# Performance work log

Hardware: AMD Instinct MI355X
Metric: run time of the kernel (lower is better)

Reference implementation:

```python
import jax, jax.numpy as jnp
import numpy as np

MARGIN = 0.3


def setup_inputs() -> dict:
    key = jax.random.key(0)
    k1, k2 = jax.random.split(key)
    N, D, C = 8192, 512, 1024
    embeddings = jax.random.normal(k1, (N, D), dtype=jnp.float32)
    labels = jax.random.randint(k2, (N,), 0, C, dtype=jnp.int64)
    return {"embeddings": embeddings, "labels": labels}


def reference(embeddings, labels):
    # L2-normalize rows, cosine distance via Gram matrix: d = 1 - e_i . e_j
    e = embeddings / jnp.linalg.norm(embeddings, axis=1, keepdims=True)
    dist = 1.0 - jnp.matmul(e, e.T)  # [N, N]

    same = labels[:, None] == labels[None, :]           # [N, N] bool
    eye = jnp.eye(labels.shape[0], dtype=bool)
    pos_mask = same & ~eye                              # positives exclude self
    neg_mask = ~same                                    # negatives

    # Batch-hard mining: hardest (farthest) positive, hardest (closest) negative
    hardest_pos = jnp.max(jnp.where(pos_mask, dist, -jnp.inf), axis=1)
    hardest_neg = jnp.min(jnp.where(neg_mask, dist, jnp.inf), axis=1)

    loss = jax.nn.relu(hardest_pos - hardest_neg + MARGIN)
    return jnp.mean(loss)
```

## Files before the change

kernel.cpp:

```cpp
#include <hip/hip_runtime.h>
#include <hip/hip_fp8.h>
#include <hip/hip_fp16.h>
#include <stdint.h>

#define MARGIN 0.3f

constexpr int N = 8192;
constexpr int D = 512;
constexpr int BM = 128, BN = 128;
constexpr int NKS = D / 64;
constexpr int NT = N / BM;
constexpr int NPAIR = NT * (NT + 1) / 2;
constexpr int WEDGE = NPAIR / 8;
constexpr float ESCALE = 16.0f;
constexpr float INV_SC2 = 1.0f / (ESCALE * ESCALE);

typedef int i32x8 __attribute__((ext_vector_type(8)));
typedef float f32x16 __attribute__((ext_vector_type(16)));
typedef __fp16 h2 __attribute__((ext_vector_type(2)));

constexpr unsigned INF2 = 0x7C007C00u;

__device__ __forceinline__ unsigned char f2fp8(float f) {
  return __hip_fp8_e4m3(f).__x;
}

__device__ __forceinline__ unsigned pkmin(unsigned a, unsigned b) {
  unsigned d;
  asm("v_pk_min_f16 %0, %1, %2" : "=v"(d) : "v"(a), "v"(b));
  return d;
}

__device__ __forceinline__ unsigned cvtpk(float lo, float hi) {
  union { h2 h; unsigned u; } cv;
  cv.h = __builtin_amdgcn_cvt_pkrtz(lo, hi);
  return cv.u;
}

__device__ __forceinline__ void pair_from_q(int q, int& ti, int& tj) {
  int SI = 0;
  while (32 * (SI + 1) * (SI + 1) + 4 * (SI + 1) <= q) ++SI;
  int r = q - (32 * SI * SI + 4 * SI);
  int i, j, SJ;
  if (r < 64 * SI) {
    SJ = r >> 6;
    int w = r & 63;
    i = w >> 3;
    j = w & 7;
  } else {
    int d = r - 64 * SI;
    SJ = SI;
    i = 0;
    while ((i + 1) * (i + 2) / 2 <= d) ++i;
    j = d - i * (i + 1) / 2;
  }
  ti = SI * 8 + i;
  tj = SJ * 8 + j;
}


__global__ __launch_bounds__(256) void normalize_rows(
    const float* __restrict__ emb, unsigned char* __restrict__ e8,
    float* __restrict__ out) {
  if (blockIdx.x == 0 && threadIdx.x == 0) out[0] = 0.f;
  const int wave = threadIdx.x >> 6, lane = threadIdx.x & 63;
  const int row = blockIdx.x * 4 + wave;
  const float4* src = (const float4*)(emb + (size_t)row * D);
  float4 x0 = src[lane];
  float4 x1 = src[lane + 64];
  float ss = x0.x * x0.x + x0.y * x0.y + x0.z * x0.z + x0.w * x0.w +
             x1.x * x1.x + x1.y * x1.y + x1.z * x1.z + x1.w * x1.w;
#pragma unroll
  for (int m = 1; m < 64; m <<= 1) ss += __shfl_xor(ss, m, 64);
  const float r = rsqrtf(ss) * ESCALE;
  union { unsigned char b[8]; uint2 u; } o;
  o.b[0] = f2fp8(x0.x * r); o.b[1] = f2fp8(x0.y * r);
  o.b[2] = f2fp8(x0.z * r); o.b[3] = f2fp8(x0.w * r);
  o.b[4] = f2fp8(x1.x * r); o.b[5] = f2fp8(x1.y * r);
  o.b[6] = f2fp8(x1.z * r); o.b[7] = f2fp8(x1.w * r);
  const int n = row & 31;
  const unsigned inner =
      (unsigned)(n * 32) + ((unsigned)((lane >> 2) & 1)) * 1024 + (lane & 3) * 8;
  const unsigned off = (unsigned)((row >> 5) * 8 + (lane >> 3)) * 2048 + inner;
  *(uint2*)(e8 + off) = o.u;
}

__global__ __launch_bounds__(256, 3) void bh_gemm_sym(
    const unsigned char* __restrict__ e8, const int* __restrict__ labels,
    unsigned* __restrict__ scr) {
  __shared__ unsigned bufR[2][128];
  __shared__ unsigned bufC[2][128];

  const int b = blockIdx.x;
  const int q = WEDGE * (b & 7) + (b >> 3);
  int ti, tj;
  pair_from_q(q, ti, tj);
  const int iBase = ti * BM, jBase = tj * BN;
  const bool diag = (ti == tj);

  const int tid = threadIdx.x;
  const int lane = tid & 63;
  const int wave = tid >> 6;
  const int wr = wave >> 1, wc = wave & 1;
  const int n = lane & 31, hi = lane >> 5;

  const unsigned char* pA0 =
      e8 + (size_t)(ti * 4 + wr * 2 + 0) * 16384 + lane * 32;
  const unsigned char* pA1 =
      e8 + (size_t)(ti * 4 + wr * 2 + 1) * 16384 + lane * 32;
  const unsigned char* pB0 =
      e8 + (size_t)(tj * 4 + wc * 2 + 0) * 16384 + lane * 32;
  const unsigned char* pB1 =
      e8 + (size_t)(tj * 4 + wc * 2 + 1) * 16384 + lane * 32;

  union Frag { i32x8 v; int4 q2[2]; };
  Frag pa[2][2], pb[2][2];

#define PREF(ph)                                       \
  {                                                    \
    pa[ph][0].q2[0] = *(const int4*)(pA0);             \
    pa[ph][0].q2[1] = *(const int4*)(pA0 + 16);        \
    pa[ph][1].q2[0] = *(const int4*)(pA1);             \
    pa[ph][1].q2[1] = *(const int4*)(pA1 + 16);        \
    pb[ph][0].q2[0] = *(const int4*)(pB0);             \
    pb[ph][0].q2[1] = *(const int4*)(pB0 + 16);        \
    pb[ph][1].q2[0] = *(const int4*)(pB1);             \
    pb[ph][1].q2[1] = *(const int4*)(pB1 + 16);        \
    pA0 += 2048; pA1 += 2048; pB0 += 2048; pB1 += 2048; \
  }

  f32x16 acc[2][2];
#pragma unroll
  for (int t = 0; t < 2; ++t)
#pragma unroll
    for (int c = 0; c < 2; ++c) acc[t][c] = (f32x16)0.0f;

  PREF(0);
  PREF(1);
#pragma unroll
  for (int T = 0; T < NKS; ++T) {
    const int ph = T & 1;
#pragma unroll
    for (int t = 0; t < 2; ++t)
#pragma unroll
      for (int c = 0; c < 2; ++c)
        acc[t][c] = __builtin_amdgcn_mfma_scale_f32_32x32x64_f8f6f4(
            pa[ph][t].v, pb[ph][c].v, acc[t][c], 0, 0,
            0, 127, 0, 127);
    if (T + 2 < NKS) PREF(ph);
  }
#undef PREF

  int lj[2];
#pragma unroll
  for (int c = 0; c < 2; ++c) lj[c] = labels[jBase + wc * 64 + c * 32 + n];

  unsigned colAcc[2] = {INF2, INF2};

#pragma unroll
  for (int t = 0; t < 2; ++t) {
    int li[16];
#pragma unroll
    for (int a = 0; a < 4; ++a) {
      int4 v = *(const int4*)(labels + iBase + wr * 64 + t * 32 + 4 * hi + 8 * a);
      li[4 * a + 0] = v.x; li[4 * a + 1] = v.y;
      li[4 * a + 2] = v.z; li[4 * a + 3] = v.w;
    }
    unsigned P[2][16];
#pragma unroll
    for (int c = 0; c < 2; ++c) {
#pragma unroll
      for (int r = 0; r < 16; ++r) {
        const float s = acc[t][c][r];
        const unsigned u = cvtpk(s, -s);
        const bool same = (li[r] == lj[c]);
        const unsigned sel = same ? 0x0000FFFFu : 0xFFFF0000u;
        unsigned p = (sel & u) | (~sel & INF2);
        if (diag) {
          const int row32 = (r & 3) + 8 * (r >> 2) + 4 * hi;
          const bool self =
              (wr * 64 + t * 32 + row32) == (wc * 64 + c * 32 + n);
          p = self ? INF2 : p;
        }
        P[c][r] = p;
      }
      if (!diag) {
        unsigned cm = P[c][0];
#pragma unroll
        for (int r = 1; r < 16; ++r) cm = pkmin(cm, P[c][r]);
        colAcc[c] = pkmin(colAcc[c], cm);
      }
    }
    unsigned m[16];
#pragma unroll
    for (int r = 0; r < 16; ++r) m[r] = pkmin(P[0][r], P[1][r]);
    unsigned w8[8];
#pragma unroll
    for (int i = 0; i < 8; ++i) {
      unsigned x = pkmin(m[2 * i],     __shfl_xor(m[2 * i],     16, 64));
      unsigned y = pkmin(m[2 * i + 1], __shfl_xor(m[2 * i + 1], 16, 64));
      w8[i] = (lane & 16) ? y : x;
    }
    unsigned w4[4];
#pragma unroll
    for (int i = 0; i < 4; ++i) {
      unsigned x = pkmin(w8[2 * i],     __shfl_xor(w8[2 * i],     8, 64));
      unsigned y = pkmin(w8[2 * i + 1], __shfl_xor(w8[2 * i + 1], 8, 64));
      w4[i] = (lane & 8) ? y : x;
    }
    unsigned w2[2];
#pragma unroll
    for (int i = 0; i < 2; ++i) {
      unsigned x = pkmin(w4[2 * i],     __shfl_xor(w4[2 * i],     4, 64));
      unsigned y = pkmin(w4[2 * i + 1], __shfl_xor(w4[2 * i + 1], 4, 64));
      w2[i] = (lane & 4) ? y : x;
    }
    unsigned x1 = pkmin(w2[0], __shfl_xor(w2[0], 2, 64));
    unsigned y1 = pkmin(w2[1], __shfl_xor(w2[1], 2, 64));
    unsigned w1 = (lane & 2) ? y1 : x1;
    w1 = pkmin(w1, __shfl_xor(w1, 1, 64));
    const int row32 = 16 * ((lane >> 1) & 1) + 8 * ((lane >> 2) & 1) + 4 * hi +
                      2 * ((lane >> 3) & 1) + ((lane >> 4) & 1);
    if ((lane & 1) == 0) bufR[wc][wr * 64 + t * 32 + row32] = w1;
  }

  if (!diag) {
#pragma unroll
    for (int c = 0; c < 2; ++c)
      colAcc[c] = pkmin(colAcc[c], __shfl_xor(colAcc[c], 32, 64));
    if (hi == 0) {
#pragma unroll
      for (int c = 0; c < 2; ++c)
        bufC[wr][wc * 64 + c * 32 + n] = colAcc[c];
    }
  }

  __syncthreads();

  if (wc == 0) {
    const int row = wr * 64 + lane;
    scr[(unsigned)(iBase + row) * 64 + tj] = pkmin(bufR[0][row], bufR[1][row]);
  }
  if (!diag && wr == 0) {
    const int col = wc * 64 + lane;
    scr[(unsigned)(jBase + col) * 64 + ti] = pkmin(bufC[0][col], bufC[1][col]);
  }
}

__global__ __launch_bounds__(256) void finalize_loss(
    const unsigned* __restrict__ scr, float* __restrict__ out) {
  const int row = blockIdx.x * 256 + threadIdx.x;
  const uint4* p = (const uint4*)(scr + (size_t)row * 64);
  unsigned mm = INF2;
#pragma unroll
  for (int i = 0; i < 16; ++i) {
    uint4 w = p[i];
    mm = pkmin(mm, pkmin(pkmin(w.x, w.y), pkmin(w.z, w.w)));
  }
  const float mn = __half2float(__ushort_as_half((unsigned short)(mm & 0xffff)));
  const float nmx = __half2float(__ushort_as_half((unsigned short)(mm >> 16)));
  float loss = (-nmx - mn) * INV_SC2 + MARGIN;
  float sum = loss > 0.f ? loss : 0.f;
#pragma unroll
  for (int m = 1; m < 64; m <<= 1) sum += __shfl_xor(sum, m, 64);
  __shared__ float ws4[4];
  const int lane = threadIdx.x & 63, wave = threadIdx.x >> 6;
  if (lane == 0) ws4[wave] = sum;
  __syncthreads();
  if (threadIdx.x == 0)
    atomicAdd(out, (ws4[0] + ws4[1] + ws4[2] + ws4[3]) * (1.0f / N));
}

extern "C" void kernel_launch(void* const* d_in, const int* in_sizes, int n_in,
                              void* d_out, int out_size, void* d_ws, size_t ws_size,
                              hipStream_t stream) {
  const float* emb = (const float*)d_in[0];
  const int* labels = (const int*)d_in[1];
  float* out = (float*)d_out;

  unsigned char* e8 = (unsigned char*)d_ws;
  unsigned* scr = (unsigned*)((char*)d_ws + (size_t)4 * 1024 * 1024);

  normalize_rows<<<N / 4, 256, 0, stream>>>(emb, e8, out);
  bh_gemm_sym<<<NPAIR, 256, 0, stream>>>(e8, labels, scr);
  finalize_loss<<<N / 256, 256, 0, stream>>>(scr, out);
}
```

Baseline: 105.9 us.

## Drop register double-buffering and fuse epilogue reductions to raise occupancy to four blocks

Raises the launch bound from three to four blocks per CU. To fit the register budget, the two-stage register prefetch of A/B fragments is replaced by per-iteration loads, and the epilogue folds row and column min-reductions into the compare loop instead of storing a 2x16 P array. The aim is to hide global-load latency through more resident waves rather than software pipelining. The risk is exposing load latency within each wave if the extra occupancy does not cover it.

```diff
diff --git a/kernel.cpp b/kernel.cpp
--- a/kernel.cpp
+++ b/kernel.cpp
@@ -85,7 +85,7 @@
   *(uint2*)(e8 + off) = o.u;
 }
 
-__global__ __launch_bounds__(256, 3) void bh_gemm_sym(
+__global__ __launch_bounds__(256, 4) void bh_gemm_sym(
     const unsigned char* __restrict__ e8, const int* __restrict__ labels,
     unsigned* __restrict__ scr) {
   __shared__ unsigned bufR[2][128];
@@ -104,30 +104,13 @@
   const int wr = wave >> 1, wc = wave & 1;
   const int n = lane & 31, hi = lane >> 5;
 
-  const unsigned char* pA0 =
-      e8 + (size_t)(ti * 4 + wr * 2 + 0) * 16384 + lane * 32;
-  const unsigned char* pA1 =
-      e8 + (size_t)(ti * 4 + wr * 2 + 1) * 16384 + lane * 32;
-  const unsigned char* pB0 =
-      e8 + (size_t)(tj * 4 + wc * 2 + 0) * 16384 + lane * 32;
-  const unsigned char* pB1 =
-      e8 + (size_t)(tj * 4 + wc * 2 + 1) * 16384 + lane * 32;
+  const unsigned char* ps[4];
+  ps[0] = e8 + (size_t)(ti * 4 + wr * 2 + 0) * 16384 + lane * 32;
+  ps[1] = e8 + (size_t)(ti * 4 + wr * 2 + 1) * 16384 + lane * 32;
+  ps[2] = e8 + (size_t)(tj * 4 + wc * 2 + 0) * 16384 + lane * 32;
+  ps[3] = e8 + (size_t)(tj * 4 + wc * 2 + 1) * 16384 + lane * 32;
 
   union Frag { i32x8 v; int4 q2[2]; };
-  Frag pa[2][2], pb[2][2];
-
-#define PREF(ph)                                       \
-  {                                                    \
-    pa[ph][0].q2[0] = *(const int4*)(pA0);             \
-    pa[ph][0].q2[1] = *(const int4*)(pA0 + 16);        \
-    pa[ph][1].q2[0] = *(const int4*)(pA1);             \
-    pa[ph][1].q2[1] = *(const int4*)(pA1 + 16);        \
-    pb[ph][0].q2[0] = *(const int4*)(pB0);             \
-    pb[ph][0].q2[1] = *(const int4*)(pB0 + 16);        \
-    pb[ph][1].q2[0] = *(const int4*)(pB1);             \
-    pb[ph][1].q2[1] = *(const int4*)(pB1 + 16);        \
-    pA0 += 2048; pA1 += 2048; pB0 += 2048; pB1 += 2048; \
-  }
 
   f32x16 acc[2][2];
 #pragma unroll
@@ -135,21 +118,22 @@
 #pragma unroll
     for (int c = 0; c < 2; ++c) acc[t][c] = (f32x16)0.0f;
 
-  PREF(0);
-  PREF(1);
 #pragma unroll
   for (int T = 0; T < NKS; ++T) {
-    const int ph = T & 1;
+    Frag fr[4];
+#pragma unroll
+    for (int s = 0; s < 4; ++s) {
+      fr[s].q2[0] = *(const int4*)(ps[s] + (size_t)T * 2048);
+      fr[s].q2[1] = *(const int4*)(ps[s] + (size_t)T * 2048 + 16);
+    }
 #pragma unroll
     for (int t = 0; t < 2; ++t)
 #pragma unroll
       for (int c = 0; c < 2; ++c)
         acc[t][c] = __builtin_amdgcn_mfma_scale_f32_32x32x64_f8f6f4(
-            pa[ph][t].v, pb[ph][c].v, acc[t][c], 0, 0,
+            fr[t].v, fr[2 + c].v, acc[t][c], 0, 0,
             0, 127, 0, 127);
-    if (T + 2 < NKS) PREF(ph);
-  }
-#undef PREF
+  }
 
   int lj[2];
 #pragma unroll
@@ -166,9 +150,10 @@
       li[4 * a + 0] = v.x; li[4 * a + 1] = v.y;
       li[4 * a + 2] = v.z; li[4 * a + 3] = v.w;
     }
-    unsigned P[2][16];
+    unsigned m[16];
 #pragma unroll
     for (int c = 0; c < 2; ++c) {
+      unsigned cm = INF2;
 #pragma unroll
       for (int r = 0; r < 16; ++r) {
         const float s = acc[t][c][r];
@@ -182,18 +167,11 @@
               (wr * 64 + t * 32 + row32) == (wc * 64 + c * 32 + n);
           p = self ? INF2 : p;
         }
-        P[c][r] = p;
+        m[r] = (c == 0) ? p : pkmin(m[r], p);
+        cm = pkmin(cm, p);
       }
-      if (!diag) {
-        unsigned cm = P[c][0];
-#pragma unroll
-        for (int r = 1; r < 16; ++r) cm = pkmin(cm, P[c][r]);
-        colAcc[c] = pkmin(colAcc[c], cm);
-      }
-    }
-    unsigned m[16];
-#pragma unroll
-    for (int r = 0; r < 16; ++r) m[r] = pkmin(P[0][r], P[1][r]);
+      if (!diag) colAcc[c] = pkmin(colAcc[c], cm);
+    }
     unsigned w8[8];
 #pragma unroll
     for (int i = 0; i < 8; ++i) {
```

Result: slower. 130.4 us (+23.2%).
